# Kernel optimization log

Measured on AMD Instinct MI355X. Metric: run time of the kernel, lower is better.

The kernel has to match this reference:

```python
import jax, jax.numpy as jnp
import numpy as np

TOP_K = 8


def setup_inputs() -> dict:
    key = jax.random.key(0)
    ks = jax.random.split(key, 5)
    B, S, H, E, I = 2, 1024, 2048, 64, 768
    return {
        "hidden_states": jax.random.normal(ks[0], (B, S, H), dtype=jnp.float32),
        "router_w": jax.random.normal(ks[1], (H, E), dtype=jnp.float32) * 0.02,
        "gate_w": jax.random.normal(ks[2], (E, H, I), dtype=jnp.float32) * 0.02,
        "up_w": jax.random.normal(ks[3], (E, H, I), dtype=jnp.float32) * 0.02,
        "down_w": jax.random.normal(ks[4], (E, I, H), dtype=jnp.float32) * 0.02,
    }


def reference(hidden_states, router_w, gate_w, up_w, down_w):
    B, S, H = hidden_states.shape
    E = router_w.shape[1]
    x = hidden_states.reshape(-1, H)                      # [T, H]
    T = x.shape[0]

    router_logits = x @ router_w                           # [T, E]
    probs = jax.nn.softmax(router_logits.astype(jnp.float32), axis=-1)
    topk_w, topk_idx = jax.lax.top_k(probs, TOP_K)         # [T, K]
    topk_w = topk_w / jnp.sum(topk_w, axis=-1, keepdims=True)  # norm_topk_prob
    topk_w = topk_w.astype(x.dtype)

    # Dense combine weights: zero for non-selected experts -> same math as the
    # gather/scatter loop, jit-friendly (no data-dependent shapes).
    combine = jnp.zeros((T, E), dtype=x.dtype)
    combine = combine.at[jnp.arange(T)[:, None], topk_idx].set(topk_w)  # [T, E]

    g = jnp.einsum('th,ehi->tei', x, gate_w)               # [T, E, I]
    u = jnp.einsum('th,ehi->tei', x, up_w)                 # [T, E, I]
    h = jax.nn.silu(g) * u                                 # SwiGLU
    out = jnp.einsum('te,tei,eih->th', combine, h, down_w)  # weighted combine

    return out.reshape(B, S, H), router_logits
```

## Files before the change

kernel.cpp:

```cpp
#include <hip/hip_runtime.h>
#include <hip/hip_bf16.h>

typedef __hip_bfloat16 bf16;
typedef short s16x8 __attribute__((ext_vector_type(8)));
typedef unsigned short u16x8 __attribute__((ext_vector_type(8)));
typedef float f32x4 __attribute__((ext_vector_type(4)));

#define T_TOK 2048
#define HDIM  2048
#define NEXP  64
#define IDIM  768
#define TOPK  8
#define OUT_OFF (T_TOK * HDIM)
#define NPAIR (T_TOK * TOPK)

#define WS_TOPK_IDX  0
#define WS_TOPK_W    (64 * 1024)
#define WS_PAIR_TOK  (128 * 1024)
#define WS_SLOT_OF   (192 * 1024)
#define WS_COUNTS    (256 * 1024)
#define WS_OFFSETS   (257 * 1024)
#define WS_CURSOR    (258 * 1024)
#define WS_H         (1024 * 1024)
#define WS_PARTIAL   (WS_H + (size_t)NPAIR * IDIM * 2)
#define WS_XB        WS_PARTIAL

__device__ __forceinline__ float bf_to_f(unsigned short u) {
    return __uint_as_float(((unsigned int)u) << 16);
}
__device__ __forceinline__ unsigned short f2bf(float f) {
    unsigned int u = __float_as_uint(f);
    unsigned int r = (u + 0x7FFFu + ((u >> 16) & 1u)) >> 16;
    return (unsigned short)r;
}
__device__ __forceinline__ unsigned cvtpk(float lo, float hi) {
    unsigned r;
    asm("v_cvt_pk_bf16_f32 %0, %1, %2" : "=v"(r) : "v"(lo), "v"(hi));
    return r;
}

typedef const __attribute__((address_space(1))) unsigned int* gas_ptr;
typedef __attribute__((address_space(3))) unsigned int* las_ptr;
__device__ __forceinline__ void gload_lds16(const void* g, void* l) {
    __builtin_amdgcn_global_load_lds((gas_ptr)g, (las_ptr)l, 16, 0, 0);
}

__global__ __launch_bounds__(256) void xbf_kernel(const float* __restrict__ x,
                                                  unsigned short* __restrict__ xb) {
    int i = blockIdx.x * 256 + threadIdx.x;
    const float4* src = (const float4*)x + (size_t)i * 2;
    float4 a = src[0], b = src[1];
    u16x8 o;
    o[0] = f2bf(a.x); o[1] = f2bf(a.y); o[2] = f2bf(a.z); o[3] = f2bf(a.w);
    o[4] = f2bf(b.x); o[5] = f2bf(b.y); o[6] = f2bf(b.z); o[7] = f2bf(b.w);
    ((u16x8*)xb)[i] = o;
}

__global__ __launch_bounds__(256) void router_kernel(
    const float* __restrict__ x, const float* __restrict__ rw,
    float* __restrict__ logits) {
    int wave = threadIdx.x >> 6;
    int lane = threadIdx.x & 63;
    int t = blockIdx.x * 4 + wave;
    const float4* x4 = (const float4*)(x + (size_t)t * HDIM);
    float acc = 0.f;
    for (int h4 = 0; h4 < HDIM / 4; ++h4) {
        float4 xv = x4[h4];
        int h = h4 * 4;
        acc = fmaf(xv.x, rw[(h + 0) * NEXP + lane], acc);
        acc = fmaf(xv.y, rw[(h + 1) * NEXP + lane], acc);
        acc = fmaf(xv.z, rw[(h + 2) * NEXP + lane], acc);
        acc = fmaf(xv.w, rw[(h + 3) * NEXP + lane], acc);
    }
    logits[t * NEXP + lane] = acc;
}

__global__ __launch_bounds__(64) void topk_kernel(
    const float* __restrict__ logits, int* __restrict__ topk_idx,
    float* __restrict__ topk_w, int* __restrict__ counts) {
    int t = blockIdx.x;
    int lane = threadIdx.x;
    float lg = logits[t * NEXP + lane];
    float mx = lg;
    for (int off = 32; off; off >>= 1) mx = fmaxf(mx, __shfl_xor(mx, off));
    float ex = expf(lg - mx);
    float sum = ex;
    for (int off = 32; off; off >>= 1) sum += __shfl_xor(sum, off);
    float prob = ex / sum;

    float pr = prob;
    float myv = 0.f;
    int myidx = 0;
    float ksum = 0.f;
    for (int k = 0; k < TOPK; ++k) {
        float v = pr;
        int idx = lane;
        for (int off = 32; off; off >>= 1) {
            float ov = __shfl_xor(v, off);
            int oi = __shfl_xor(idx, off);
            if (ov > v || (ov == v && oi < idx)) { v = ov; idx = oi; }
        }
        ksum += v;
        if (lane == k) { myidx = idx; myv = v; }
        if (lane == idx) pr = -1.f;
    }
    if (lane < TOPK) {
        topk_idx[t * TOPK + lane] = myidx;
        topk_w[t * TOPK + lane] = myv / ksum;
        atomicAdd(&counts[myidx], 1);
    }
}

__global__ __launch_bounds__(64) void scan_kernel(
    const int* __restrict__ counts, int* __restrict__ offsets, int* __restrict__ cursor) {
    int lane = threadIdx.x;
    int c = counts[lane];
    int incl = c;
    for (int off = 1; off < 64; off <<= 1) {
        int tt = __shfl_up(incl, off);
        if (lane >= off) incl += tt;
    }
    offsets[lane] = incl - c;
    if (lane == 63) offsets[64] = incl;
    cursor[lane] = 0;
}

__global__ __launch_bounds__(256) void scatter_kernel(
    const int* __restrict__ topk_idx, const int* __restrict__ offsets,
    int* __restrict__ cursor, int* __restrict__ pair_token, int* __restrict__ slot_of) {
    int i = blockIdx.x * 256 + threadIdx.x;
    if (i >= NPAIR) return;
    int t = i >> 3;
    int e = topk_idx[i];
    int pos = atomicAdd(&cursor[e], 1);
    int slot = offsets[e] + pos;
    pair_token[slot] = t;
    slot_of[i] = slot;
}

#define BM   128
#define BKS  64
#define NZG  6
#define NZD  8
#define NKG  (HDIM / BKS)
#define NKD  (IDIM / BKS)

__global__ __launch_bounds__(1024, 4) void gateup_mfma(
    const unsigned short* __restrict__ xb, const float* __restrict__ gate_w,
    const float* __restrict__ up_w, const int* __restrict__ offsets,
    const int* __restrict__ pair_token, unsigned short* __restrict__ hbuf) {
    int id = blockIdx.x;
    int xcd = id & 7, rid = id >> 3;
    int ntile = rid % NZG;
    int y = (rid / NZG) & 1;
    int e = (rid / (2 * NZG)) * 8 + xcd;
    int off = offsets[e];
    int cnt = offsets[e + 1] - off;
    if (cnt <= 0) return;

    __shared__ unsigned short As[2][BM * BKS];
    __shared__ unsigned short Bgu[2][256 * BKS];
    __shared__ int toks[BM];

    int tid = threadIdx.x;
    int lane = tid & 63;
    int w = tid >> 6;
    int wr = w & 1, wc = w >> 1;
    int l15 = lane & 15, lg4 = lane >> 4;

    int mat = tid >> 9;
    int s = tid & 511;
    int nI2 = s & 63, kC = s >> 6;
    int brow0 = mat * 128 + nI2 * 2;
    int bslot = (kC ^ (nI2 & 7)) * 8;
    const float* bsrc = (mat ? up_w : gate_w) + (size_t)e * HDIM * IDIM
                        + (size_t)(kC * 8) * IDIM + ntile * 128 + nI2 * 2;

    int arow = tid >> 3;
    int ajx = (tid & 7) ^ (arow & 7);

    for (int mt = y; mt * BM < cnt; mt += 2) {
        int m0 = mt * BM;
        if (tid < BM) {
            int p = m0 + tid;
            toks[tid] = pair_token[off + (p < cnt ? p : 0)];
        }
        __syncthreads();
        const unsigned short* aq = xb + (size_t)toks[arow] * HDIM + ajx * 8;
        f32x4 accg[4] = {};
        f32x4 accu[4] = {};

        gload_lds16(aq, &As[0][tid * 8]);
        float2 Bv[8];
        #pragma unroll
        for (int i = 0; i < 8; ++i)
            Bv[i] = *(const float2*)(bsrc + (size_t)i * IDIM);

        for (int ks = 0; ks < NKG; ++ks) {
            int p = ks & 1;
            {
                uint4 w0, w1;
                w0.x = cvtpk(Bv[0].x, Bv[1].x); w0.y = cvtpk(Bv[2].x, Bv[3].x);
                w0.z = cvtpk(Bv[4].x, Bv[5].x); w0.w = cvtpk(Bv[6].x, Bv[7].x);
                w1.x = cvtpk(Bv[0].y, Bv[1].y); w1.y = cvtpk(Bv[2].y, Bv[3].y);
                w1.z = cvtpk(Bv[4].y, Bv[5].y); w1.w = cvtpk(Bv[6].y, Bv[7].y);
                *(uint4*)&Bgu[p][brow0 * BKS + bslot] = w0;
                *(uint4*)&Bgu[p][(brow0 + 1) * BKS + bslot] = w1;
            }
            __syncthreads();
            if (ks + 1 < NKG) {
                int h1 = (ks + 1) * BKS;
                gload_lds16(aq + h1, &As[p ^ 1][tid * 8]);
                #pragma unroll
                for (int i = 0; i < 8; ++i)
                    Bv[i] = *(const float2*)(bsrc + (size_t)(h1 + i) * IDIM);
            }
            #pragma unroll
            for (int kk = 0; kk < 2; ++kk) {
                int jk = kk * 4 + lg4;
                s16x8 a[4], bg, bu;
                #pragma unroll
                for (int mr = 0; mr < 4; ++mr) {
                    int r = wr * 64 + mr * 16 + l15;
                    a[mr] = *(const s16x8*)&As[p][r * BKS + ((jk ^ (r & 7)) * 8)];
                }
                int rg = wc * 16 + l15;
                int ru = 128 + rg;
                bg = *(const s16x8*)&Bgu[p][rg * BKS + ((jk ^ ((rg >> 1) & 7)) * 8)];
                bu = *(const s16x8*)&Bgu[p][ru * BKS + ((jk ^ ((ru >> 1) & 7)) * 8)];
                #pragma unroll
                for (int mr = 0; mr < 4; ++mr) {
                    accg[mr] = __builtin_amdgcn_mfma_f32_16x16x32_bf16(a[mr], bg, accg[mr], 0, 0, 0);
                    accu[mr] = __builtin_amdgcn_mfma_f32_16x16x32_bf16(a[mr], bu, accu[mr], 0, 0, 0);
                }
            }
        }

        int col = ntile * 128 + wc * 16 + l15;
        #pragma unroll
        for (int mr = 0; mr < 4; ++mr) {
            #pragma unroll
            for (int reg = 0; reg < 4; ++reg) {
                int r = m0 + wr * 64 + mr * 16 + lg4 * 4 + reg;
                if (r < cnt) {
                    float g = accg[mr][reg];
                    float u = accu[mr][reg];
                    float hv = (g / (1.f + __expf(-g))) * u;
                    hbuf[(size_t)(off + r) * IDIM + col] = f2bf(hv);
                }
            }
        }
        __syncthreads();
    }
}

__global__ __launch_bounds__(1024, 4) void down_mfma(
    const unsigned short* __restrict__ hbuf, const float* __restrict__ down_w,
    const int* __restrict__ offsets, unsigned short* __restrict__ partial) {
    int id = blockIdx.x;
    int xcd = id & 7, rid = id >> 3;
    int ntile = rid % NZD;
    int y = (rid / NZD) & 1;
    int e = (rid / (2 * NZD)) * 8 + xcd;
    int off = offsets[e];
    int cnt = offsets[e + 1] - off;
    if (cnt <= 0) return;

    __shared__ unsigned short As[2][BM * BKS];
    __shared__ unsigned short Bd[2][256 * BKS];

    int tid = threadIdx.x;
    int lane = tid & 63;
    int w = tid >> 6;
    int wr = w & 1, wc = w >> 1;
    int l15 = lane & 15, lg4 = lane >> 4;

    int nI2 = tid & 127, kC = tid >> 7;
    int brow0 = nI2 * 2;
    int bslot = (kC ^ (nI2 & 7)) * 8;
    const float* bsrc = down_w + (size_t)e * IDIM * HDIM
                        + (size_t)(kC * 8) * HDIM + ntile * 256 + nI2 * 2;

    int arow = tid >> 3;
    int ajx = (tid & 7) ^ (arow & 7);

    for (int mt = y; mt * BM < cnt; mt += 2) {
        int m0 = mt * BM;
        __syncthreads();
        int rr = m0 + arow;
        if (rr >= cnt) rr = cnt - 1;
        const unsigned short* aq = hbuf + (size_t)(off + rr) * IDIM + ajx * 8;
        f32x4 acc[4][2] = {};

        gload_lds16(aq, &As[0][tid * 8]);
        float2 Bv[8];
        #pragma unroll
        for (int i = 0; i < 8; ++i)
            Bv[i] = *(const float2*)(bsrc + (size_t)i * HDIM);

        for (int ks = 0; ks < NKD; ++ks) {
            int p = ks & 1;
            {
                uint4 w0, w1;
                w0.x = cvtpk(Bv[0].x, Bv[1].x); w0.y = cvtpk(Bv[2].x, Bv[3].x);
                w0.z = cvtpk(Bv[4].x, Bv[5].x); w0.w = cvtpk(Bv[6].x, Bv[7].x);
                w1.x = cvtpk(Bv[0].y, Bv[1].y); w1.y = cvtpk(Bv[2].y, Bv[3].y);
                w1.z = cvtpk(Bv[4].y, Bv[5].y); w1.w = cvtpk(Bv[6].y, Bv[7].y);
                *(uint4*)&Bd[p][brow0 * BKS + bslot] = w0;
                *(uint4*)&Bd[p][(brow0 + 1) * BKS + bslot] = w1;
            }
            __syncthreads();
            if (ks + 1 < NKD) {
                int k1 = (ks + 1) * BKS;
                gload_lds16(aq + k1, &As[p ^ 1][tid * 8]);
                #pragma unroll
                for (int i = 0; i < 8; ++i)
                    Bv[i] = *(const float2*)(bsrc + (size_t)(k1 + i) * HDIM);
            }
            #pragma unroll
            for (int kk = 0; kk < 2; ++kk) {
                int jk = kk * 4 + lg4;
                s16x8 a[4], b[2];
                #pragma unroll
                for (int mr = 0; mr < 4; ++mr) {
                    int r = wr * 64 + mr * 16 + l15;
                    a[mr] = *(const s16x8*)&As[p][r * BKS + ((jk ^ (r & 7)) * 8)];
                }
                #pragma unroll
                for (int nr = 0; nr < 2; ++nr) {
                    int row = wc * 32 + nr * 16 + l15;
                    b[nr] = *(const s16x8*)&Bd[p][row * BKS + ((jk ^ ((row >> 1) & 7)) * 8)];
                }
                #pragma unroll
                for (int mr = 0; mr < 4; ++mr)
                    #pragma unroll
                    for (int nr = 0; nr < 2; ++nr)
                        acc[mr][nr] = __builtin_amdgcn_mfma_f32_16x16x32_bf16(
                            a[mr], b[nr], acc[mr][nr], 0, 0, 0);
            }
        }

        #pragma unroll
        for (int mr = 0; mr < 4; ++mr)
            #pragma unroll
            for (int nr = 0; nr < 2; ++nr) {
                int col = ntile * 256 + wc * 32 + nr * 16 + l15;
                #pragma unroll
                for (int reg = 0; reg < 4; ++reg) {
                    int r = m0 + wr * 64 + mr * 16 + lg4 * 4 + reg;
                    if (r < cnt)
                        partial[(size_t)(off + r) * HDIM + col] = f2bf(acc[mr][nr][reg]);
                }
            }
        __syncthreads();
    }
}

__global__ __launch_bounds__(256) void reduce_kernel(
    const unsigned short* __restrict__ partial, const int* __restrict__ slot_of,
    const float* __restrict__ topk_w, float* __restrict__ out) {
    int t = blockIdx.x;
    int j8 = threadIdx.x * 8;
    __shared__ int ss[8];
    __shared__ float sw[8];
    if (threadIdx.x < 8) {
        ss[threadIdx.x] = slot_of[t * TOPK + threadIdx.x];
        sw[threadIdx.x] = topk_w[t * TOPK + threadIdx.x];
    }
    __syncthreads();
    float acc[8] = {};
    #pragma unroll
    for (int k = 0; k < TOPK; ++k) {
        u16x8 v = *(const u16x8*)&partial[(size_t)ss[k] * HDIM + j8];
        float w = sw[k];
        #pragma unroll
        for (int i = 0; i < 8; ++i)
            acc[i] = fmaf(w, bf_to_f((unsigned short)v[i]), acc[i]);
    }
    float4 o0 = {acc[0], acc[1], acc[2], acc[3]};
    float4 o1 = {acc[4], acc[5], acc[6], acc[7]};
    *(float4*)&out[(size_t)t * HDIM + j8] = o0;
    *(float4*)&out[(size_t)t * HDIM + j8 + 4] = o1;
}

extern "C" void kernel_launch(void* const* d_in, const int* in_sizes, int n_in,
                              void* d_out, int out_size, void* d_ws, size_t ws_size,
                              hipStream_t stream) {
    const float* x  = (const float*)d_in[0];
    const float* rw = (const float*)d_in[1];
    const float* gw = (const float*)d_in[2];
    const float* uw = (const float*)d_in[3];
    const float* dw = (const float*)d_in[4];
    float* out = (float*)d_out;
    float* logits = out + OUT_OFF;

    char* ws = (char*)d_ws;
    int*   topk_idx   = (int*)(ws + WS_TOPK_IDX);
    float* topk_w     = (float*)(ws + WS_TOPK_W);
    int*   pair_token = (int*)(ws + WS_PAIR_TOK);
    int*   slot_of    = (int*)(ws + WS_SLOT_OF);
    int*   counts     = (int*)(ws + WS_COUNTS);
    int*   offsets    = (int*)(ws + WS_OFFSETS);
    int*   cursor     = (int*)(ws + WS_CURSOR);
    unsigned short* hbuf    = (unsigned short*)(ws + WS_H);
    unsigned short* partial = (unsigned short*)(ws + WS_PARTIAL);
    unsigned short* xb      = (unsigned short*)(ws + WS_XB);

    hipMemsetAsync(counts, 0, NEXP * sizeof(int), stream);
    xbf_kernel<<<T_TOK * HDIM / (256 * 8), 256, 0, stream>>>(x, xb);
    router_kernel<<<T_TOK / 4, 256, 0, stream>>>(x, rw, logits);
    topk_kernel<<<T_TOK, 64, 0, stream>>>(logits, topk_idx, topk_w, counts);
    scan_kernel<<<1, 64, 0, stream>>>(counts, offsets, cursor);
    scatter_kernel<<<NPAIR / 256, 256, 0, stream>>>(topk_idx, offsets, cursor, pair_token, slot_of);
    gateup_mfma<<<NEXP * 2 * NZG, 1024, 0, stream>>>(xb, gw, uw, offsets, pair_token, hbuf);
    down_mfma<<<NEXP * 2 * NZD, 1024, 0, stream>>>(hbuf, dw, offsets, partial);
    reduce_kernel<<<dim3(T_TOK, 1), 256, 0, stream>>>(partial, slot_of, topk_w, out);
}
```

Baseline: 726.5 us.

## Double M tile to 256 rows and drop the two-way M split per expert

Expert GEMMs now use 256-row M tiles. Each block loads two A row sets and the waves are rearranged as 4x4, so each wave computes a 4x2 (gate/up) or 4x4 (down) MFMA tile. Each fp32 weight tile is converted to bf16 once per 256 tokens instead of once per 128, which halves redundant weight streaming and conversion. The grid shrinks by half, so fewer blocks run and register pressure rises from the larger accumulator arrays, which may hurt occupancy.

```diff
diff --git a/kernel.cpp b/kernel.cpp
--- a/kernel.cpp
+++ b/kernel.cpp
@@ -138,7 +138,7 @@
     slot_of[i] = slot;
 }
 
-#define BM   128
+#define BM   256
 #define BKS  64
 #define NZG  6
 #define NZD  8
@@ -150,10 +150,9 @@
     const float* __restrict__ up_w, const int* __restrict__ offsets,
     const int* __restrict__ pair_token, unsigned short* __restrict__ hbuf) {
     int id = blockIdx.x;
-    int xcd = id & 7, rid = id >> 3;
-    int ntile = rid % NZG;
-    int y = (rid / NZG) & 1;
-    int e = (rid / (2 * NZG)) * 8 + xcd;
+    int b = id & 7, g = id >> 3;
+    int ntile = g % NZG;
+    int e = b + 8 * (g / NZG);
     int off = offsets[e];
     int cnt = offsets[e + 1] - off;
     if (cnt <= 0) return;
@@ -165,7 +164,7 @@
     int tid = threadIdx.x;
     int lane = tid & 63;
     int w = tid >> 6;
-    int wr = w & 1, wc = w >> 1;
+    int wr = w & 3, wc = w >> 2;
     int l15 = lane & 15, lg4 = lane >> 4;
 
     int mat = tid >> 9;
@@ -179,18 +178,21 @@
     int arow = tid >> 3;
     int ajx = (tid & 7) ^ (arow & 7);
 
-    for (int mt = y; mt * BM < cnt; mt += 2) {
+    for (int mt = 0; mt * BM < cnt; ++mt) {
         int m0 = mt * BM;
         if (tid < BM) {
             int p = m0 + tid;
             toks[tid] = pair_token[off + (p < cnt ? p : 0)];
         }
         __syncthreads();
-        const unsigned short* aq = xb + (size_t)toks[arow] * HDIM + ajx * 8;
-        f32x4 accg[4] = {};
-        f32x4 accu[4] = {};
-
-        gload_lds16(aq, &As[0][tid * 8]);
+        const unsigned short* aq[2];
+        aq[0] = xb + (size_t)toks[arow] * HDIM + ajx * 8;
+        aq[1] = xb + (size_t)toks[arow + 128] * HDIM + ajx * 8;
+        f32x4 accg[4][2] = {};
+        f32x4 accu[4][2] = {};
+
+        gload_lds16(aq[0], &As[0][tid * 8]);
+        gload_lds16(aq[1], &As[0][(1024 + tid) * 8]);
         float2 Bv[8];
         #pragma unroll
         for (int i = 0; i < 8; ++i)
@@ -210,7 +212,8 @@
             __syncthreads();
             if (ks + 1 < NKG) {
                 int h1 = (ks + 1) * BKS;
-                gload_lds16(aq + h1, &As[p ^ 1][tid * 8]);
+                gload_lds16(aq[0] + h1, &As[p ^ 1][tid * 8]);
+                gload_lds16(aq[1] + h1, &As[p ^ 1][(1024 + tid) * 8]);
                 #pragma unroll
                 for (int i = 0; i < 8; ++i)
                     Bv[i] = *(const float2*)(bsrc + (size_t)(h1 + i) * IDIM);
@@ -218,38 +221,45 @@
             #pragma unroll
             for (int kk = 0; kk < 2; ++kk) {
                 int jk = kk * 4 + lg4;
-                s16x8 a[4], bg, bu;
+                s16x8 a[4], bg[2], bu[2];
                 #pragma unroll
                 for (int mr = 0; mr < 4; ++mr) {
                     int r = wr * 64 + mr * 16 + l15;
                     a[mr] = *(const s16x8*)&As[p][r * BKS + ((jk ^ (r & 7)) * 8)];
                 }
-                int rg = wc * 16 + l15;
-                int ru = 128 + rg;
-                bg = *(const s16x8*)&Bgu[p][rg * BKS + ((jk ^ ((rg >> 1) & 7)) * 8)];
-                bu = *(const s16x8*)&Bgu[p][ru * BKS + ((jk ^ ((ru >> 1) & 7)) * 8)];
-                #pragma unroll
-                for (int mr = 0; mr < 4; ++mr) {
-                    accg[mr] = __builtin_amdgcn_mfma_f32_16x16x32_bf16(a[mr], bg, accg[mr], 0, 0, 0);
-                    accu[mr] = __builtin_amdgcn_mfma_f32_16x16x32_bf16(a[mr], bu, accu[mr], 0, 0, 0);
-                }
+                #pragma unroll
+                for (int nr = 0; nr < 2; ++nr) {
+                    int rg = wc * 32 + nr * 16 + l15;
+                    int ru = 128 + rg;
+                    bg[nr] = *(const s16x8*)&Bgu[p][rg * BKS + ((jk ^ ((rg >> 1) & 7)) * 8)];
+                    bu[nr] = *(const s16x8*)&Bgu[p][ru * BKS + ((jk ^ ((ru >> 1) & 7)) * 8)];
+                }
+                #pragma unroll
+                for (int mr = 0; mr < 4; ++mr)
+                    #pragma unroll
+                    for (int nr = 0; nr < 2; ++nr) {
+                        accg[mr][nr] = __builtin_amdgcn_mfma_f32_16x16x32_bf16(a[mr], bg[nr], accg[mr][nr], 0, 0, 0);
+                        accu[mr][nr] = __builtin_amdgcn_mfma_f32_16x16x32_bf16(a[mr], bu[nr], accu[mr][nr], 0, 0, 0);
+                    }
             }
         }
 
-        int col = ntile * 128 + wc * 16 + l15;
         #pragma unroll
-        for (int mr = 0; mr < 4; ++mr) {
+        for (int mr = 0; mr < 4; ++mr)
             #pragma unroll
-            for (int reg = 0; reg < 4; ++reg) {
-                int r = m0 + wr * 64 + mr * 16 + lg4 * 4 + reg;
-                if (r < cnt) {
-                    float g = accg[mr][reg];
-                    float u = accu[mr][reg];
-                    float hv = (g / (1.f + __expf(-g))) * u;
-                    hbuf[(size_t)(off + r) * IDIM + col] = f2bf(hv);
-                }
-            }
-        }
+            for (int nr = 0; nr < 2; ++nr) {
+                int col = ntile * 128 + wc * 32 + nr * 16 + l15;
+                #pragma unroll
+                for (int reg = 0; reg < 4; ++reg) {
+                    int r = m0 + wr * 64 + mr * 16 + lg4 * 4 + reg;
+                    if (r < cnt) {
+                        float gv = accg[mr][nr][reg];
+                        float uv = accu[mr][nr][reg];
+                        float hv = (gv / (1.f + __expf(-gv))) * uv;
+                        hbuf[(size_t)(off + r) * IDIM + col] = f2bf(hv);
+                    }
+                }
+            }
         __syncthreads();
     }
 }
@@ -258,10 +268,9 @@
     const unsigned short* __restrict__ hbuf, const float* __restrict__ down_w,
     const int* __restrict__ offsets, unsigned short* __restrict__ partial) {
     int id = blockIdx.x;
-    int xcd = id & 7, rid = id >> 3;
-    int ntile = rid % NZD;
-    int y = (rid / NZD) & 1;
-    int e = (rid / (2 * NZD)) * 8 + xcd;
+    int b = id & 7, g = id >> 3;
+    int ntile = g % NZD;
+    int e = b + 8 * (g / NZD);
     int off = offsets[e];
     int cnt = offsets[e + 1] - off;
     if (cnt <= 0) return;
@@ -272,7 +281,7 @@
     int tid = threadIdx.x;
     int lane = tid & 63;
     int w = tid >> 6;
-    int wr = w & 1, wc = w >> 1;
+    int wr = w & 3, wc = w >> 2;
     int l15 = lane & 15, lg4 = lane >> 4;
 
     int nI2 = tid & 127, kC = tid >> 7;
@@ -284,15 +293,18 @@
     int arow = tid >> 3;
     int ajx = (tid & 7) ^ (arow & 7);
 
-    for (int mt = y; mt * BM < cnt; mt += 2) {
+    for (int mt = 0; mt * BM < cnt; ++mt) {
         int m0 = mt * BM;
         __syncthreads();
-        int rr = m0 + arow;
-        if (rr >= cnt) rr = cnt - 1;
-        const unsigned short* aq = hbuf + (size_t)(off + rr) * IDIM + ajx * 8;
-        f32x4 acc[4][2] = {};
-
-        gload_lds16(aq, &As[0][tid * 8]);
+        int r0 = m0 + arow;       if (r0 >= cnt) r0 = cnt - 1;
+        int r1 = m0 + arow + 128; if (r1 >= cnt) r1 = cnt - 1;
+        const unsigned short* aq[2];
+        aq[0] = hbuf + (size_t)(off + r0) * IDIM + ajx * 8;
+        aq[1] = hbuf + (size_t)(off + r1) * IDIM + ajx * 8;
+        f32x4 acc[4][4] = {};
+
+        gload_lds16(aq[0], &As[0][tid * 8]);
+        gload_lds16(aq[1], &As[0][(1024 + tid) * 8]);
         float2 Bv[8];
         #pragma unroll
         for (int i = 0; i < 8; ++i)
@@ -312,7 +324,8 @@
             __syncthreads();
             if (ks + 1 < NKD) {
                 int k1 = (ks + 1) * BKS;
-                gload_lds16(aq + k1, &As[p ^ 1][tid * 8]);
+                gload_lds16(aq[0] + k1, &As[p ^ 1][tid * 8]);
+                gload_lds16(aq[1] + k1, &As[p ^ 1][(1024 + tid) * 8]);
                 #pragma unroll
                 for (int i = 0; i < 8; ++i)
                     Bv[i] = *(const float2*)(bsrc + (size_t)(k1 + i) * HDIM);
@@ -320,31 +333,31 @@
             #pragma unroll
             for (int kk = 0; kk < 2; ++kk) {
                 int jk = kk * 4 + lg4;
-                s16x8 a[4], b[2];
+                s16x8 a[4], bb[4];
                 #pragma unroll
                 for (int mr = 0; mr < 4; ++mr) {
                     int r = wr * 64 + mr * 16 + l15;
                     a[mr] = *(const s16x8*)&As[p][r * BKS + ((jk ^ (r & 7)) * 8)];
                 }
                 #pragma unroll
-                for (int nr = 0; nr < 2; ++nr) {
-                    int row = wc * 32 + nr * 16 + l15;
-                    b[nr] = *(const s16x8*)&Bd[p][row * BKS + ((jk ^ ((row >> 1) & 7)) * 8)];
+                for (int nr = 0; nr < 4; ++nr) {
+                    int row = wc * 64 + nr * 16 + l15;
+                    bb[nr] = *(const s16x8*)&Bd[p][row * BKS + ((jk ^ ((row >> 1) & 7)) * 8)];
                 }
                 #pragma unroll
                 for (int mr = 0; mr < 4; ++mr)
                     #pragma unroll
-                    for (int nr = 0; nr < 2; ++nr)
+                    for (int nr = 0; nr < 4; ++nr)
                         acc[mr][nr] = __builtin_amdgcn_mfma_f32_16x16x32_bf16(
-                            a[mr], b[nr], acc[mr][nr], 0, 0, 0);
+                            a[mr], bb[nr], acc[mr][nr], 0, 0, 0);
             }
         }
 
         #pragma unroll
         for (int mr = 0; mr < 4; ++mr)
             #pragma unroll
-            for (int nr = 0; nr < 2; ++nr) {
-                int col = ntile * 256 + wc * 32 + nr * 16 + l15;
+            for (int nr = 0; nr < 4; ++nr) {
+                int col = ntile * 256 + wc * 64 + nr * 16 + l15;
                 #pragma unroll
                 for (int reg = 0; reg < 4; ++reg) {
                     int r = m0 + wr * 64 + mr * 16 + lg4 * 4 + reg;
@@ -412,7 +425,7 @@
     topk_kernel<<<T_TOK, 64, 0, stream>>>(logits, topk_idx, topk_w, counts);
     scan_kernel<<<1, 64, 0, stream>>>(counts, offsets, cursor);
     scatter_kernel<<<NPAIR / 256, 256, 0, stream>>>(topk_idx, offsets, cursor, pair_token, slot_of);
-    gateup_mfma<<<NEXP * 2 * NZG, 1024, 0, stream>>>(xb, gw, uw, offsets, pair_token, hbuf);
-    down_mfma<<<NEXP * 2 * NZD, 1024, 0, stream>>>(hbuf, dw, offsets, partial);
+    gateup_mfma<<<NEXP * NZG, 1024, 0, stream>>>(xb, gw, uw, offsets, pair_token, hbuf);
+    down_mfma<<<NEXP * NZD, 1024, 0, stream>>>(hbuf, dw, offsets, partial);
     reduce_kernel<<<dim3(T_TOK, 1), 256, 0, stream>>>(partial, slot_of, topk_w, out);
 }
```

Result: no change. 734.0 us (+1.0%).
